# Kernel tuning notes

Measured on AMD Instinct MI355X. Metric: run time of the kernel, lower is better.

The kernel has to match this reference:

```python
import jax, jax.numpy as jnp
import numpy as np

K = 3      # kernel_size
S = 2      # stride
EPS = 1e-5 # BatchNorm eps


def setup_inputs() -> dict:
    key = jax.random.key(0)
    ks = jax.random.split(key, 6)
    B, C, H, W = 8, 256, 128, 128
    k2 = K * K
    return {
        "x": jax.random.normal(ks[0], (B, C, H, W), jnp.float32),
        "w_conv": jax.random.normal(ks[1], (k2, C, K, K), jnp.float32) * 0.05,
        "bn_gamma": jnp.ones((k2,), jnp.float32),
        "bn_beta": jnp.zeros((k2,), jnp.float32),
        "bn_mean": jax.random.normal(ks[2], (k2,), jnp.float32) * 0.1,
        "bn_var": jnp.ones((k2,), jnp.float32),
        "ch_w1": jax.random.normal(ks[3], (C // 4, C), jnp.float32) * 0.05,
        "ch_w2": jax.random.normal(ks[4], (C, C // 4), jnp.float32) * 0.05,
    }


def reference(x, w_conv, bn_gamma, bn_beta, bn_mean, bn_var, ch_w1, ch_w2):
    b, c, h, w = x.shape
    oh = (h - 1) // S + 1
    ow = (w - 1) // S + 1
    # weight_net: strided KxK conv (C -> k2) + eval-mode BatchNorm
    wlog = jax.lax.conv_general_dilated(
        x, w_conv, window_strides=(S, S), padding=((1, 1), (1, 1)),
        dimension_numbers=("NCHW", "OIHW", "NCHW"))  # (b, k2, oh, ow)
    scale = bn_gamma / jnp.sqrt(bn_var + EPS)
    wlog = (wlog - bn_mean[None, :, None, None]) * scale[None, :, None, None] \
        + bn_beta[None, :, None, None]
    # channel_net: GAP -> 1x1 conv -> relu -> 1x1 conv (all bias-free)
    gap = x.mean(axis=(2, 3))                      # (b, c)
    ch = jax.nn.relu(gap @ ch_w1.T) @ ch_w2.T      # (b, c)
    # per-pixel, per-channel logits over the k^2 taps; softmax over taps
    logits = wlog[:, None] * ch[:, :, None, None, None]  # (b, c, k2, oh, ow)
    attn = jax.nn.softmax(logits, axis=2)
    # unfold: reflect pad then KxK patches with stride S (tap order row-major,
    # matching torch unfold(2,.).unfold(3,.) and the k2->(k,k) reshape)
    px = jnp.pad(x, ((0, 0), (0, 0), (1, 1), (1, 1)), mode="reflect")
    taps = []
    for di in range(K):
        for dj in range(K):
            taps.append(px[:, :, di:di + (oh - 1) * S + 1:S,
                           dj:dj + (ow - 1) * S + 1:S])
    patches = jnp.stack(taps, axis=2)              # (b, c, k2, oh, ow)
    return (attn * patches).sum(axis=2)            # (b, c, oh, ow)
```

## Files before the change

### kernel.cpp

```cpp
#include <hip/hip_runtime.h>
#include <hip/hip_bf16.h>


#define EPS 1e-5f
#define CH_SPLIT 8
#define CH_PER_WAVE 8

__global__ __launch_bounds__(256) void prep_init_kernel(
    const float* __restrict__ wconv, const float* __restrict__ gamma,
    const float* __restrict__ beta, const float* __restrict__ mean,
    const float* __restrict__ var, float* __restrict__ wt,
    float* __restrict__ gap, float* __restrict__ wlog) {
  const int blk = blockIdx.x;
  if (blk < 1536) {
    float biasv[9];
    #pragma unroll
    for (int t = 0; t < 9; ++t)
      biasv[t] = beta[t] - mean[t] * gamma[t] * rsqrtf(var[t] + EPS);
    const int idx = blk * 256 + threadIdx.x;
    const int t = idx % 12;
    wlog[idx] = (t < 9) ? biasv[t] : 0.f;
  } else {
    const int c = threadIdx.x;
    #pragma unroll
    for (int t = 0; t < 9; ++t) {
      float sc = gamma[t] * rsqrtf(var[t] + EPS);
      #pragma unroll
      for (int ki = 0; ki < 3; ++ki)
        #pragma unroll
        for (int kj = 0; kj < 3; ++kj)
          wt[c * 84 + ki * 28 + t * 3 + kj] =
              wconv[((size_t)t * 256 + c) * 9 + ki * 3 + kj] * sc;
    }
    #pragma unroll
    for (int ki = 0; ki < 3; ++ki) wt[c * 84 + ki * 28 + 27] = 0.f;
    #pragma unroll
    for (int k = 0; k < 8; ++k) gap[k * 256 + c] = 0.f;
  }
}

__global__ __launch_bounds__(256, 4) void conv_kernel(
    const float* __restrict__ x, const float* __restrict__ wt,
    float* __restrict__ wlog, float* __restrict__ gap) {
  const int j = threadIdx.x & 63;
  const int wv = threadIdx.x >> 6;
  const int i0 = blockIdx.x * 4;
  const int b = blockIdx.y;
  const int z = blockIdx.z;
  const int cbase = __builtin_amdgcn_readfirstlane((z * 4 + wv) * CH_PER_WAVE);

  float acc[4][9];
  #pragma unroll
  for (int ri = 0; ri < 4; ++ri)
    #pragma unroll
    for (int t = 0; t < 9; ++t) acc[ri][t] = 0.f;

  const float* xb = x + ((size_t)b * 256 + cbase) * 16384;
  const float* wcb = wt + (size_t)cbase * 84;
  const int h0 = 2 * i0 - 1;

  for (int c = 0; c < CH_PER_WAVE; ++c, xb += 16384, wcb += 84) {
    float2 v[9];
    #pragma unroll
    for (int r = 0; r < 9; ++r) {
      const int hh = h0 + r;
      if ((unsigned)hh < 128u)
        v[r] = *(const float2*)(xb + hh * 128 + 2 * j);
      else
        v[r] = make_float2(0.f, 0.f);
    }
    float lf[9];
    #pragma unroll
    for (int r = 0; r < 9; ++r) {
      float t = __shfl_up(v[r].y, 1, 64);
      lf[r] = (j == 0) ? 0.f : t;
    }
    float gs = 0.f;
    #pragma unroll
    for (int r = 1; r < 9; ++r) gs += v[r].x + v[r].y;
    #pragma unroll
    for (int off = 32; off; off >>= 1) gs += __shfl_xor(gs, off, 64);
    if (j == 0) atomicAdd(&gap[b * 256 + cbase + c], gs);

    #pragma unroll
    for (int ki = 0; ki < 3; ++ki) {
      float4 wk[7];
      const float4* wq = (const float4*)(wcb + ki * 28);
      #pragma unroll
      for (int q = 0; q < 7; ++q) wk[q] = wq[q];
      const float* w = (const float*)wk;
      #pragma unroll
      for (int ri = 0; ri < 4; ++ri) {
        const int r = 2 * ri + ki;
        const float x0 = lf[r], x1 = v[r].x, x2 = v[r].y;
        #pragma unroll
        for (int t = 0; t < 9; ++t) {
          float a = acc[ri][t];
          a = fmaf(x0, w[t * 3 + 0], a);
          a = fmaf(x1, w[t * 3 + 1], a);
          a = fmaf(x2, w[t * 3 + 2], a);
          acc[ri][t] = a;
        }
      }
    }
  }

  __shared__ float red[4][64][9];
  #pragma unroll
  for (int ri = 0; ri < 4; ++ri) {
    __syncthreads();
    #pragma unroll
    for (int t = 0; t < 9; ++t) red[wv][j][t] = acc[ri][t];
    __syncthreads();
    const size_t rowpos = ((size_t)b * 64 + (i0 + ri)) * 64;
    for (int idx = threadIdx.x; idx < 576; idx += 256) {
      const int jj = idx / 9, tt = idx - jj * 9;
      float s =
          red[0][jj][tt] + red[1][jj][tt] + red[2][jj][tt] + red[3][jj][tt];
      atomicAdd(&wlog[(rowpos + jj) * 12 + tt], s);
    }
  }
}

__global__ __launch_bounds__(256) void chnet_kernel(
    const float* __restrict__ gap, const float* __restrict__ w1,
    const float* __restrict__ w2, float* __restrict__ ch) {
  const int b = blockIdx.x;
  __shared__ float g[256];
  __shared__ float h[64];
  const int t = threadIdx.x;
  g[t] = gap[b * 256 + t] * (1.f / 16384.f);
  __syncthreads();
  if (t < 64) {
    float s = 0.f;
    const float* w = w1 + t * 256;
    for (int c = 0; c < 256; ++c) s += g[c] * w[c];
    h[t] = fmaxf(s, 0.f);
  }
  __syncthreads();
  float s = 0.f;
  const float* w = w2 + t * 64;
  #pragma unroll 4
  for (int j = 0; j < 64; ++j) s += h[j] * w[j];
  ch[b * 256 + t] = s;
}

__global__ __launch_bounds__(256) void final_kernel(
    const float* __restrict__ x, const float* __restrict__ wlog,
    const float* __restrict__ ch, float* __restrict__ out) {
  const int j = threadIdx.x & 63;
  const int il = threadIdx.x >> 6;
  const int i = blockIdx.x * 4 + il;
  const int b = blockIdx.y;
  const int c0 = blockIdx.z * 32;

  const size_t pos = ((size_t)b * 64 + i) * 64 + j;
  const float4* wp = (const float4*)(wlog + pos * 12);
  float4 wa = wp[0], wb = wp[1], wcv = wp[2];
  const float wl[9] = {wa.x, wa.y, wa.z, wa.w, wb.x, wb.y, wb.z, wb.w, wcv.x};

  const float* chp = ch + b * 256 + c0;
  const float* xp0 = x + ((size_t)b * 256 + c0) * 16384;
  float* op = out + ((size_t)b * 256 + c0) * 4096 + i * 64 + j;

  for (int c = 0; c < 32; ++c) {
    const float chv = chp[c];
    const float* xp = xp0 + (size_t)c * 16384;

    float2 v0, v1, v2;
    {
      int hh = 2 * i - 1;
      hh = hh < 0 ? -hh : hh;
      v0 = *(const float2*)(xp + hh * 128 + 2 * j);
      v1 = *(const float2*)(xp + (2 * i) * 128 + 2 * j);
      v2 = *(const float2*)(xp + (2 * i + 1) * 128 + 2 * j);
    }

    float lg[9], m = -3.4e38f;
    #pragma unroll
    for (int t = 0; t < 9; ++t) {
      lg[t] = wl[t] * chv;
      m = fmaxf(m, lg[t]);
    }
    float e[9], s = 0.f;
    #pragma unroll
    for (int t = 0; t < 9; ++t) {
      e[t] = __expf(lg[t] - m);
      s += e[t];
    }
    const float inv = 1.f / s;

    float l0 = __shfl_up(v0.y, 1, 64);
    float l1 = __shfl_up(v1.y, 1, 64);
    float l2 = __shfl_up(v2.y, 1, 64);
    float acc = e[0] * l0 + e[1] * v0.x + e[2] * v0.y;
    acc += e[3] * l1 + e[4] * v1.x + e[5] * v1.y;
    acc += e[6] * l2 + e[7] * v2.x + e[8] * v2.y;

    op[(size_t)c * 4096] = acc * inv;
  }
}

extern "C" void kernel_launch(void* const* d_in, const int* in_sizes, int n_in,
                              void* d_out, int out_size, void* d_ws,
                              size_t ws_size, hipStream_t stream) {
  const float* x = (const float*)d_in[0];
  const float* w_conv = (const float*)d_in[1];
  const float* bn_gamma = (const float*)d_in[2];
  const float* bn_beta = (const float*)d_in[3];
  const float* bn_mean = (const float*)d_in[4];
  const float* bn_var = (const float*)d_in[5];
  const float* ch_w1 = (const float*)d_in[6];
  const float* ch_w2 = (const float*)d_in[7];
  float* out = (float*)d_out;

  float* wsf = (float*)d_ws;
  float* gap = wsf;
  float* ch = wsf + 2048;
  float* wt = wsf + 4096;
  float* wlog = wsf + 25600;

  prep_init_kernel<<<1537, 256, 0, stream>>>(w_conv, bn_gamma, bn_beta,
                                             bn_mean, bn_var, wt, gap, wlog);
  conv_kernel<<<dim3(16, 8, CH_SPLIT), 256, 0, stream>>>(x, wt, wlog, gap);
  chnet_kernel<<<8, 256, 0, stream>>>(gap, ch_w1, ch_w2, ch);
  final_kernel<<<dim3(16, 8, 8), 256, 0, stream>>>(x, wlog, ch, out);
}
```

Baseline: 86.11 us.

## Replace wlog atomics with per-split partial buffers and a fused reduce pass

```diff
diff --git a/kernel.cpp b/kernel.cpp
--- a/kernel.cpp
+++ b/kernel.cpp
@@ -5,49 +5,54 @@
 #define EPS 1e-5f
 #define CH_SPLIT 8
 #define CH_PER_WAVE 8
-
-__global__ __launch_bounds__(256) void prep_init_kernel(
+#define WLOG_N 393216
+
+__global__ __launch_bounds__(256) void prep_kernel(
     const float* __restrict__ wconv, const float* __restrict__ gamma,
     const float* __restrict__ beta, const float* __restrict__ mean,
     const float* __restrict__ var, float* __restrict__ wt,
-    float* __restrict__ gap, float* __restrict__ wlog) {
-  const int blk = blockIdx.x;
-  if (blk < 1536) {
-    float biasv[9];
-    #pragma unroll
-    for (int t = 0; t < 9; ++t)
-      biasv[t] = beta[t] - mean[t] * gamma[t] * rsqrtf(var[t] + EPS);
-    const int idx = blk * 256 + threadIdx.x;
-    const int t = idx % 12;
-    wlog[idx] = (t < 9) ? biasv[t] : 0.f;
-  } else {
-    const int c = threadIdx.x;
-    #pragma unroll
-    for (int t = 0; t < 9; ++t) {
-      float sc = gamma[t] * rsqrtf(var[t] + EPS);
+    float* __restrict__ bias, float* __restrict__ gap) {
+  const int c = threadIdx.x;
+  #pragma unroll
+  for (int t = 0; t < 9; ++t) {
+    float sc = gamma[t] * rsqrtf(var[t] + EPS);
+    #pragma unroll
+    for (int ki = 0; ki < 3; ++ki)
       #pragma unroll
-      for (int ki = 0; ki < 3; ++ki)
-        #pragma unroll
-        for (int kj = 0; kj < 3; ++kj)
-          wt[c * 84 + ki * 28 + t * 3 + kj] =
-              wconv[((size_t)t * 256 + c) * 9 + ki * 3 + kj] * sc;
-    }
-    #pragma unroll
-    for (int ki = 0; ki < 3; ++ki) wt[c * 84 + ki * 28 + 27] = 0.f;
-    #pragma unroll
-    for (int k = 0; k < 8; ++k) gap[k * 256 + c] = 0.f;
-  }
+      for (int kj = 0; kj < 3; ++kj)
+        wt[c * 84 + ki * 28 + t * 3 + kj] =
+            wconv[((size_t)t * 256 + c) * 9 + ki * 3 + kj] * sc;
+  }
+  #pragma unroll
+  for (int ki = 0; ki < 3; ++ki) wt[c * 84 + ki * 28 + 27] = 0.f;
+  #pragma unroll
+  for (int k = 0; k < 8; ++k) gap[k * 256 + c] = 0.f;
+  if (c < 9) bias[c] = beta[c] - mean[c] * gamma[c] * rsqrtf(var[c] + EPS);
+  else if (c < 16) bias[c] = 0.f;
 }
 
 __global__ __launch_bounds__(256, 4) void conv_kernel(
     const float* __restrict__ x, const float* __restrict__ wt,
-    float* __restrict__ wlog, float* __restrict__ gap) {
+    float* __restrict__ wlogp, float* __restrict__ gap) {
   const int j = threadIdx.x & 63;
   const int wv = threadIdx.x >> 6;
   const int i0 = blockIdx.x * 4;
   const int b = blockIdx.y;
   const int z = blockIdx.z;
-  const int cbase = __builtin_amdgcn_readfirstlane((z * 4 + wv) * CH_PER_WAVE);
+
+  __shared__ float sw[2688];
+  __shared__ float red[4][64][9];
+
+  {
+    const float4* src = (const float4*)(wt + (size_t)z * 32 * 84);
+    float4* dst = (float4*)sw;
+    #pragma unroll
+    for (int k = 0; k < 3; ++k) {
+      int idx = k * 256 + threadIdx.x;
+      if (idx < 672) dst[idx] = src[idx];
+    }
+  }
+  __syncthreads();
 
   float acc[4][9];
   #pragma unroll
@@ -55,11 +60,12 @@
     #pragma unroll
     for (int t = 0; t < 9; ++t) acc[ri][t] = 0.f;
 
+  const int cbase = z * 32 + wv * CH_PER_WAVE;
   const float* xb = x + ((size_t)b * 256 + cbase) * 16384;
-  const float* wcb = wt + (size_t)cbase * 84;
+  const float* swb = sw + (wv * CH_PER_WAVE) * 84;
   const int h0 = 2 * i0 - 1;
 
-  for (int c = 0; c < CH_PER_WAVE; ++c, xb += 16384, wcb += 84) {
+  for (int c = 0; c < CH_PER_WAVE; ++c, xb += 16384) {
     float2 v[9];
     #pragma unroll
     for (int r = 0; r < 9; ++r) {
@@ -82,6 +88,7 @@
     for (int off = 32; off; off >>= 1) gs += __shfl_xor(gs, off, 64);
     if (j == 0) atomicAdd(&gap[b * 256 + cbase + c], gs);
 
+    const float* wcb = swb + c * 84;
     #pragma unroll
     for (int ki = 0; ki < 3; ++ki) {
       float4 wk[7];
@@ -105,7 +112,7 @@
     }
   }
 
-  __shared__ float red[4][64][9];
+  float* wzp = wlogp + (size_t)z * WLOG_N;
   #pragma unroll
   for (int ri = 0; ri < 4; ++ri) {
     __syncthreads();
@@ -113,36 +120,57 @@
     for (int t = 0; t < 9; ++t) red[wv][j][t] = acc[ri][t];
     __syncthreads();
     const size_t rowpos = ((size_t)b * 64 + (i0 + ri)) * 64;
-    for (int idx = threadIdx.x; idx < 576; idx += 256) {
-      const int jj = idx / 9, tt = idx - jj * 9;
-      float s =
-          red[0][jj][tt] + red[1][jj][tt] + red[2][jj][tt] + red[3][jj][tt];
-      atomicAdd(&wlog[(rowpos + jj) * 12 + tt], s);
-    }
-  }
-}
-
-__global__ __launch_bounds__(256) void chnet_kernel(
-    const float* __restrict__ gap, const float* __restrict__ w1,
-    const float* __restrict__ w2, float* __restrict__ ch) {
-  const int b = blockIdx.x;
+    float* wp = wzp + rowpos * 12;
+    for (int idx = threadIdx.x; idx < 768; idx += 256) {
+      const int jj = idx / 12, tt = idx - jj * 12;
+      float s = 0.f;
+      if (tt < 9)
+        s = red[0][jj][tt] + red[1][jj][tt] + red[2][jj][tt] + red[3][jj][tt];
+      wp[idx] = s;
+    }
+  }
+}
+
+__global__ __launch_bounds__(256) void reduce_chnet_kernel(
+    const float* __restrict__ wlogp, const float* __restrict__ bias,
+    float* __restrict__ wlog, const float* __restrict__ gap,
+    const float* __restrict__ w1, const float* __restrict__ w2,
+    float* __restrict__ ch) {
   __shared__ float g[256];
   __shared__ float h[64];
-  const int t = threadIdx.x;
-  g[t] = gap[b * 256 + t] * (1.f / 16384.f);
-  __syncthreads();
-  if (t < 64) {
+  const int blk = blockIdx.x;
+  if (blk < 384) {
+    const int i4 = blk * 256 + threadIdx.x;
+    float4 s = make_float4(0.f, 0.f, 0.f, 0.f);
+    #pragma unroll
+    for (int zz = 0; zz < 8; ++zz) {
+      float4 p = *(const float4*)(wlogp + (size_t)zz * WLOG_N + (size_t)i4 * 4);
+      s.x += p.x; s.y += p.y; s.z += p.z; s.w += p.w;
+    }
+    const int base = i4 * 4;
+    s.x += bias[(base + 0) % 12];
+    s.y += bias[(base + 1) % 12];
+    s.z += bias[(base + 2) % 12];
+    s.w += bias[(base + 3) % 12];
+    *(float4*)(wlog + base) = s;
+  } else {
+    const int b = blk - 384;
+    const int t = threadIdx.x;
+    g[t] = gap[b * 256 + t] * (1.f / 16384.f);
+    __syncthreads();
+    if (t < 64) {
+      float s = 0.f;
+      const float* w = w1 + t * 256;
+      for (int c = 0; c < 256; ++c) s += g[c] * w[c];
+      h[t] = fmaxf(s, 0.f);
+    }
+    __syncthreads();
     float s = 0.f;
-    const float* w = w1 + t * 256;
-    for (int c = 0; c < 256; ++c) s += g[c] * w[c];
-    h[t] = fmaxf(s, 0.f);
-  }
-  __syncthreads();
-  float s = 0.f;
-  const float* w = w2 + t * 64;
-  #pragma unroll 4
-  for (int j = 0; j < 64; ++j) s += h[j] * w[j];
-  ch[b * 256 + t] = s;
+    const float* w = w2 + t * 64;
+    #pragma unroll 4
+    for (int jj = 0; jj < 64; ++jj) s += h[jj] * w[jj];
+    ch[b * 256 + t] = s;
+  }
 }
 
 __global__ __launch_bounds__(256) void final_kernel(
@@ -152,7 +180,7 @@
   const int il = threadIdx.x >> 6;
   const int i = blockIdx.x * 4 + il;
   const int b = blockIdx.y;
-  const int c0 = blockIdx.z * 32;
+  const int c0 = blockIdx.z * 16;
 
   const size_t pos = ((size_t)b * 64 + i) * 64 + j;
   const float4* wp = (const float4*)(wlog + pos * 12);
@@ -163,7 +191,7 @@
   const float* xp0 = x + ((size_t)b * 256 + c0) * 16384;
   float* op = out + ((size_t)b * 256 + c0) * 4096 + i * 64 + j;
 
-  for (int c = 0; c < 32; ++c) {
+  for (int c = 0; c < 16; ++c) {
     const float chv = chp[c];
     const float* xp = xp0 + (size_t)c * 16384;
 
@@ -217,12 +245,15 @@
   float* wsf = (float*)d_ws;
   float* gap = wsf;
   float* ch = wsf + 2048;
-  float* wt = wsf + 4096;
-  float* wlog = wsf + 25600;
-
-  prep_init_kernel<<<1537, 256, 0, stream>>>(w_conv, bn_gamma, bn_beta,
-                                             bn_mean, bn_var, wt, gap, wlog);
-  conv_kernel<<<dim3(16, 8, CH_SPLIT), 256, 0, stream>>>(x, wt, wlog, gap);
-  chnet_kernel<<<8, 256, 0, stream>>>(gap, ch_w1, ch_w2, ch);
-  final_kernel<<<dim3(16, 8, 8), 256, 0, stream>>>(x, wlog, ch, out);
-}
+  float* bias = wsf + 4096;
+  float* wt = wsf + 4112;
+  float* wlog = wsf + 25616;
+  float* wlogp = wsf + 418832;
+
+  prep_kernel<<<1, 256, 0, stream>>>(w_conv, bn_gamma, bn_beta, bn_mean,
+                                     bn_var, wt, bias, gap);
+  conv_kernel<<<dim3(16, 8, CH_SPLIT), 256, 0, stream>>>(x, wt, wlogp, gap);
+  reduce_chnet_kernel<<<392, 256, 0, stream>>>(wlogp, bias, wlog, gap, ch_w1,
+                                               ch_w2, ch);
+  final_kernel<<<dim3(16, 8, 16), 256, 0, stream>>>(x, wlog, ch, out);
+}
```

New measurement: 79.33 us. 7.9% less time.
